# Kernel tuning notes

Measured on AMD Instinct MI355X. Metric: run time of the kernel, lower is better.

## Reference

```python
import jax, jax.numpy as jnp
import numpy as np


def gelu(x):
    # custom GELU classes in such repos typically implement the tanh approximation
    return jax.nn.gelu(x, approximate=True)


def setup_inputs() -> dict:
    key = jax.random.key(0)
    ks = jax.random.split(key, 16)
    B, N1, N2, D, H = 4, 1024, 1024, 256, 4
    prev = jax.random.normal(ks[0], (B, N1, D), dtype=jnp.float32)
    curr = jax.random.normal(ks[1], (B, N2, D), dtype=jnp.float32)
    edges = jax.random.randint(ks[2], (B, N1, N2), 0, 2).astype(jnp.int32)

    def lin(k, fan_in, fan_out):
        kw, kb = jax.random.split(k)
        s = 1.0 / np.sqrt(fan_in)
        W = jax.random.uniform(kw, (fan_in, fan_out), jnp.float32, -s, s)
        b = jax.random.uniform(kb, (fan_out,), jnp.float32, -s, s)
        return W, b

    W_pre, b_pre = lin(ks[3], D, 6)
    W_cur, b_cur = lin(ks[4], D, 6)
    W_fuse, b_fuse = lin(ks[5], 12, 4)
    W_ffn, b_ffn = lin(ks[6], 12, 8)
    W_fcc, b_fcc = lin(ks[7], 8, H)
    W_fcg, b_fcg = lin(ks[8], 8, D)
    return {"prev": prev, "curr": curr, "edges": edges,
            "W_pre": W_pre, "b_pre": b_pre, "W_cur": W_cur, "b_cur": b_cur,
            "W_fuse": W_fuse, "b_fuse": b_fuse, "W_ffn": W_ffn, "b_ffn": b_ffn,
            "W_fcc": W_fcc, "b_fcc": b_fcc, "W_fcg": W_fcg, "b_fcg": b_fcg}


def reference(prev, curr, edges, W_pre, b_pre, W_cur, b_cur,
              W_fuse, b_fuse, W_ffn, b_ffn, W_fcc, b_fcc, W_fcg, b_fcg):
    B, N1, D = prev.shape
    N2 = curr.shape[1]
    H = W_fcc.shape[1]
    Dh = D // H
    mask = edges != 0                                   # [B,N1,N2]

    bt_pre = prev @ W_pre + b_pre                       # [B,N1,6]
    bt_cur = curr @ W_cur + b_cur                       # [B,N2,6]
    pair = jnp.concatenate([
        jnp.broadcast_to(bt_pre[:, :, None, :], (B, N1, N2, 6)),
        jnp.broadcast_to(bt_cur[:, None, :, :], (B, N1, N2, 6))], axis=-1)
    c = gelu(pair) @ W_fuse + b_fuse                    # [B,N1,N2,4]
    c = jnp.where(mask[..., None], c, 0.0)

    e1 = (jnp.sum(edges, axis=1) + 1).astype(c.dtype)   # [B,N2]
    d = jnp.sum(c, axis=1)[:, None] / e1[:, None, :, None]
    d = jnp.broadcast_to(d, c.shape)
    e = jnp.broadcast_to(jnp.max(c, axis=1)[:, None], c.shape)
    fused = gelu(jnp.concatenate([c, d, e], axis=-1)) @ W_ffn + b_ffn  # [B,N1,N2,8]

    att = gelu(fused) @ W_fcc + b_fcc                   # [B,N1,N2,H]
    att = jnp.transpose(att, (0, 2, 1, 3))              # [B,N2,N1,H]
    maskT = jnp.transpose(mask, (0, 2, 1))              # [B,N2,N1]
    logits = jnp.where(maskT[..., None], att, -9e15)
    p = jax.nn.softmax(logits, axis=2)                  # softmax over N1 per head
    p = jnp.where(maskT[..., None], p, 0.0)
    # per-head aggregation: head i uses prev columns [i*Dh, (i+1)*Dh)
    res = jnp.einsum('bmnh,bnhd->bmhd', p, prev.reshape(B, N1, H, Dh)).reshape(B, N2, D)

    fused_m = jnp.where(mask[..., None], fused, 0.0)
    g = jnp.sum(fused_m, axis=1) / e1[..., None]        # [B,N2,8]
    return res + gelu(g) @ W_fcg + b_fcg                # [B,N2,D]
```

## Files before the change

kernel.cpp:

```cpp
#include <hip/hip_runtime.h>


using bf16x8 = __attribute__((ext_vector_type(8))) short;
using f32x4  = __attribute__((ext_vector_type(4))) float;
typedef float v2f __attribute__((ext_vector_type(2)));

__device__ __forceinline__ v2f pk_fma(v2f a, v2f b, v2f c){
    return __builtin_elementwise_fma(a, b, c);
}

__device__ __forceinline__ float gelu_f(float x){
    float x2 = x*x;
    float tt = x * __builtin_fmaf(0.044715f, x2, 1.0f);
    float e  = exp2f(-2.3022082f * tt);
    return x * __builtin_amdgcn_rcpf(1.0f + e);
}

__device__ __forceinline__ v2f gelu2(v2f x){
    v2f x2 = x*x;
    v2f tt = x * pk_fma((v2f){0.044715f,0.044715f}, x2, (v2f){1.0f,1.0f});
    float e0 = exp2f(-2.3022082f * tt[0]);
    float e1 = exp2f(-2.3022082f * tt[1]);
    v2f r = { __builtin_amdgcn_rcpf(1.0f + e0),
              __builtin_amdgcn_rcpf(1.0f + e1) };
    return x * r;
}

__device__ __forceinline__ unsigned short f2bf(float f){
    unsigned int u = __float_as_uint(f);
    u += 0x7FFFu + ((u >> 16) & 1u);
    return (unsigned short)(u >> 16);
}

__global__ __launch_bounds__(256) void k_prevT(
    const float* __restrict__ prev, unsigned short* __restrict__ prevT)
{
    int bid = blockIdx.x;
    int b  = bid >> 6;
    int it = (bid >> 2) & 15;
    int dt = bid & 3;
    int i0 = it*64, d0 = dt*64;
    int t = threadIdx.x;
    int col = t & 63, rw = t >> 6;
    __shared__ float tile[64][65];
    #pragma unroll
    for (int r = 0; r < 16; ++r){
        int row = rw + 4*r;
        tile[row][col] = prev[((size_t)b*1024 + i0 + row)*256 + d0 + col];
    }
    __syncthreads();
    #pragma unroll
    for (int r = 0; r < 16; ++r){
        int drow = rw + 4*r;
        prevT[((size_t)b*256 + d0 + drow)*1024 + i0 + col] = f2bf(tile[col][drow]);
    }
}

__global__ __launch_bounds__(256) void k_rows(
    const float* __restrict__ prev, const float* __restrict__ curr,
    const float* __restrict__ W_pre, const float* __restrict__ b_pre,
    const float* __restrict__ W_cur, const float* __restrict__ b_cur,
    const float* __restrict__ W_fuse, const float* __restrict__ b_fuse,
    float* __restrict__ u_ws, float* __restrict__ v_ws)
{
    int gid  = blockIdx.x * 256 + threadIdx.x;
    int wave = gid >> 6;
    int lane = threadIdx.x & 63;
    bool isPrev = wave < 4096;
    int row = isPrev ? wave : (wave - 4096);
    const float* xrow = (isPrev ? prev : curr) + (size_t)row * 256;
    const float* W  = isPrev ? W_pre : W_cur;
    const float* bv = isPrev ? b_pre : b_cur;

    float4 x4 = *reinterpret_cast<const float4*>(xrow + lane*4);
    const float* Wl = W + lane*24;
    float p[6];
    #pragma unroll
    for (int k=0;k<6;++k)
        p[k] = x4.x*Wl[k] + x4.y*Wl[6+k] + x4.z*Wl[12+k] + x4.w*Wl[18+k];
    #pragma unroll
    for (int off=32; off>=1; off>>=1){
        #pragma unroll
        for (int k=0;k<6;++k) p[k] += __shfl_xor(p[k], off, 64);
    }
    if (lane == 0){
        float g[6];
        #pragma unroll
        for(int k=0;k<6;++k) g[k] = gelu_f(p[k] + bv[k]);
        int rb = isPrev ? 0 : 6;
        float o[4];
        #pragma unroll
        for(int kk=0;kk<4;++kk){
            float a = isPrev ? 0.0f : b_fuse[kk];
            #pragma unroll
            for(int k=0;k<6;++k) a += g[k]*W_fuse[(rb+k)*4+kk];
            o[kk]=a;
        }
        float* dst = (isPrev ? u_ws : v_ws) + (size_t)row*4;
        *reinterpret_cast<float4*>(dst) = make_float4(o[0],o[1],o[2],o[3]);
    }
}

__global__ __launch_bounds__(256) void k_cols(
    const int* __restrict__ edges,
    const float* __restrict__ u_ws, const float* __restrict__ v_ws,
    const float* __restrict__ W_ffn, const float* __restrict__ b_ffn,
    float* __restrict__ Gd_ws, float* __restrict__ cnt_ws)
{
    int b  = blockIdx.x >> 6;
    int j0 = (blockIdx.x & 63) * 16;
    int t  = threadIdx.x;
    int jq = t & 3, sl = t >> 2;
    const int*   eb = edges + (size_t)b*1048576 + j0 + jq*4;
    const float* ub = u_ws + (size_t)b*4096;

    int   cnt[4] = {0,0,0,0};
    float S[4][4] = {{0.f}};
    float M[4][4];
    #pragma unroll
    for (int q=0;q<4;++q)
        #pragma unroll
        for (int k=0;k<4;++k) M[q][k] = -3.4e38f;

    #pragma unroll 4
    for (int ii=0; ii<16; ++ii){
        int i = sl*16 + ii;
        int4   e4 = *reinterpret_cast<const int4*>(eb + (size_t)i*1024);
        float4 u4 = *reinterpret_cast<const float4*>(ub + i*4);
        float uu[4] = {u4.x,u4.y,u4.z,u4.w};
        int   ee[4] = {e4.x,e4.y,e4.z,e4.w};
        #pragma unroll
        for (int q=0;q<4;++q){
            bool mk = ee[q]!=0;
            cnt[q] += mk ? 1 : 0;
            #pragma unroll
            for (int k=0;k<4;++k){
                S[q][k] += mk ? uu[k] : 0.0f;
                M[q][k]  = mk ? fmaxf(M[q][k],uu[k]) : M[q][k];
            }
        }
    }
    __shared__ float rS[64][16][4];
    __shared__ float rM[64][16][4];
    __shared__ int   rC[64][16];
    #pragma unroll
    for (int q=0;q<4;++q){
        int c = jq*4+q;
        #pragma unroll
        for (int k=0;k<4;++k){ rS[sl][c][k]=S[q][k]; rM[sl][c][k]=M[q][k]; }
        rC[sl][c]=cnt[q];
    }
    __syncthreads();
    float aS[4], aM[4]; int aC=0; int c2=0, hf=0;
    if (t < 128){
        c2 = t & 15; hf = t >> 4;
        #pragma unroll
        for(int k=0;k<4;++k){ aS[k]=0.f; aM[k]=-3.4e38f; }
        for (int s2=hf*8; s2<hf*8+8; ++s2){
            aC += rC[s2][c2];
            #pragma unroll
            for(int k=0;k<4;++k){ aS[k]+=rS[s2][c2][k]; aM[k]=fmaxf(aM[k],rM[s2][c2][k]); }
        }
    }
    __syncthreads();
    if (t < 128){
        rC[hf][c2]=aC;
        #pragma unroll
        for(int k=0;k<4;++k){ rS[hf][c2][k]=aS[k]; rM[hf][c2][k]=aM[k]; }
    }
    __syncthreads();
    if (t < 16){
        int cc=0; float Sa[4]={0,0,0,0};
        float Ma[4]={-3.4e38f,-3.4e38f,-3.4e38f,-3.4e38f};
        for (int s2=0;s2<8;++s2){
            cc += rC[s2][t];
            #pragma unroll
            for(int k=0;k<4;++k){ Sa[k]+=rS[s2][t][k]; Ma[k]=fmaxf(Ma[k],rM[s2][t][k]); }
        }
        size_t cj = (size_t)b*1024 + j0 + t;
        float4 v4 = *reinterpret_cast<const float4*>(v_ws + cj*4);
        float vv[4]={v4.x,v4.y,v4.z,v4.w};
        float cf = (float)cc, e1 = cf + 1.0f;
        float gd[4], ge[4];
        #pragma unroll
        for(int k=0;k<4;++k){
            float dk = (Sa[k] + cf*vv[k]) / e1;
            float ek;
            if (cc == 0) ek = 0.0f;
            else { float m1 = Ma[k]+vv[k]; ek = (cc < 1024) ? fmaxf(m1, 0.0f) : m1; }
            gd[k]=gelu_f(dk); ge[k]=gelu_f(ek);
        }
        #pragma unroll
        for(int kk=0;kk<8;++kk){
            float a = b_ffn[kk];
            #pragma unroll
            for(int k=0;k<4;++k)
                a += gd[k]*W_ffn[(4+k)*8+kk] + ge[k]*W_ffn[(8+k)*8+kk];
            Gd_ws[cj*8+kk]=a;
        }
        cnt_ws[cj]=cf;
    }
}

template<int SPLIT>
__global__ __launch_bounds__(256) void k_main(
    const unsigned short* __restrict__ prevT, const int* __restrict__ edges,
    const float* __restrict__ u_ws, const float* __restrict__ v_ws,
    const float* __restrict__ Gd_ws,
    const float* __restrict__ W_ffn, const float* __restrict__ W_fcc,
    const float* __restrict__ b_fcc,
    float* __restrict__ Pws, float* __restrict__ Sws, float* __restrict__ Tws)
{
    const int RPB = 1024/SPLIT;
    int bid = blockIdx.x;
    int sp  = bid & (SPLIT-1);
    int jt  = (bid / SPLIT) & 127;
    int b   = bid / (SPLIT*128);
    int j0  = jt*8;
    int t   = threadIdx.x;
    int lane = t & 63;
    int wv   = t >> 6;
    int jl_w = t & 7, il_w = t >> 3;

    __shared__ unsigned short wA[4096];
    __shared__ __align__(16) float sU[64][4];
    __shared__ float sV[8][4];
    __shared__ float sGd[8][8];
    __shared__ float sT4[256][4];

    if (t < 32) (&sV[0][0])[t]  = v_ws[((size_t)b*1024 + j0)*4 + t];
    if (t < 64) (&sGd[0][0])[t] = Gd_ws[((size_t)b*1024 + j0)*8 + t];
    {
        unsigned int* wz = (unsigned int*)wA;
        #pragma unroll
        for (int z=0; z<8; ++z) wz[t + z*256] = 0u;
    }

    const float LOG2E = 1.4426950408889634f;
    v2f W4p[4][4], Wfcp[8][2], bfcp[2];
    #pragma unroll
    for(int k=0;k<4;++k)
        #pragma unroll
        for(int q=0;q<4;++q)
            W4p[k][q] = (v2f){W_ffn[k*8+2*q], W_ffn[k*8+2*q+1]};
    #pragma unroll
    for(int kk=0;kk<8;++kk)
        #pragma unroll
        for(int p2=0;p2<2;++p2)
            Wfcp[kk][p2] = (v2f){W_fcc[kk*4+2*p2]*LOG2E, W_fcc[kk*4+2*p2+1]*LOG2E};
    #pragma unroll
    for(int p2=0;p2<2;++p2)
        bfcp[p2] = (v2f){b_fcc[2*p2]*LOG2E, b_fcc[2*p2+1]*LOG2E};

    f32x4 accm[4];
    #pragma unroll
    for (int tile=0;tile<4;++tile) accm[tile] = (f32x4){0.f,0.f,0.f,0.f};
    f32x4 accs = (f32x4){0.f,0.f,0.f,0.f};
    bf16x8 onesB;
    #pragma unroll
    for (int e=0;e<8;++e) onesB[e] = (short)0x3F80;
    v2f Tp01 = {0,0}, Tp23 = {0,0};

    const int* ebase = edges + (size_t)b*1048576 + j0;
    const int NCH = RPB/64;
    const int base_i0 = sp*RPB;

    __syncthreads();
    float4 v4p = *reinterpret_cast<const float4*>(&sV[jl_w][0]);
    float4 gd0 = *reinterpret_cast<const float4*>(&sGd[jl_w][0]);
    float4 gd1 = *reinterpret_cast<const float4*>(&sGd[jl_w][4]);

    int arow = lane & 15, kgrp = lane >> 4;
    int aoff0 = (((wv*16 + arow)*64 + kgrp*8)*2) ^ ((arow & 7) << 4);
    int aoff1 = aoff0 ^ 64;
    const unsigned short* pTbase = prevT
        + ((size_t)b*256 + wv*64 + arow)*1024 + base_i0 + kgrp*8;

    float su_r = u_ws[((size_t)b*1024 + base_i0)*4 + t];
    int   egr0 = ebase[(size_t)(base_i0+il_w   )*1024 + jl_w];
    int   egr1 = ebase[(size_t)(base_i0+il_w+32)*1024 + jl_w];

    for (int cc=0; cc<NCH; ++cc){
        (&sU[0][0])[t] = su_r;
        __syncthreads();

        int eg2[2] = {egr0, egr1};
        #pragma unroll
        for (int r=0;r<2;++r){
            int il = il_w + 32*r;
            int eg = eg2[r];
            float4 u4 = *reinterpret_cast<const float4*>(&sU[il][0]);
            v2f g01 = gelu2((v2f){u4.x + v4p.x, u4.y + v4p.y});
            v2f g23 = gelu2((v2f){u4.z + v4p.z, u4.w + v4p.w});
            float m = eg ? 1.0f : 0.0f;
            v2f mm = {m, m};
            Tp01 = pk_fma(mm, g01, Tp01);
            Tp23 = pk_fma(mm, g23, Tp23);
            v2f a0 = {gd0.x, gd0.y}, a1 = {gd0.z, gd0.w};
            v2f a2 = {gd1.x, gd1.y}, a3 = {gd1.z, gd1.w};
            v2f G0 = {g01[0], g01[0]}, G1 = {g01[1], g01[1]};
            v2f G2 = {g23[0], g23[0]}, G3 = {g23[1], g23[1]};
            a0 = pk_fma(G0, W4p[0][0], a0); a1 = pk_fma(G0, W4p[0][1], a1);
            a2 = pk_fma(G0, W4p[0][2], a2); a3 = pk_fma(G0, W4p[0][3], a3);
            a0 = pk_fma(G1, W4p[1][0], a0); a1 = pk_fma(G1, W4p[1][1], a1);
            a2 = pk_fma(G1, W4p[1][2], a2); a3 = pk_fma(G1, W4p[1][3], a3);
            a0 = pk_fma(G2, W4p[2][0], a0); a1 = pk_fma(G2, W4p[2][1], a1);
            a2 = pk_fma(G2, W4p[2][2], a2); a3 = pk_fma(G2, W4p[2][3], a3);
            a0 = pk_fma(G3, W4p[3][0], a0); a1 = pk_fma(G3, W4p[3][1], a1);
            a2 = pk_fma(G3, W4p[3][2], a2); a3 = pk_fma(G3, W4p[3][3], a3);
            v2f f01 = gelu2(a0), f23 = gelu2(a1);
            v2f f45 = gelu2(a2), f67 = gelu2(a3);
            v2f L01 = bfcp[0], L23 = bfcp[1];
            float fv[8] = {f01[0],f01[1],f23[0],f23[1],f45[0],f45[1],f67[0],f67[1]};
            #pragma unroll
            for (int kk=0;kk<8;++kk){
                v2f F = {fv[kk], fv[kk]};
                L01 = pk_fma(F, Wfcp[kk][0], L01);
                L23 = pk_fma(F, Wfcp[kk][1], L23);
            }
            float lg[4] = {L01[0], L01[1], L23[0], L23[1]};
            int low = ((jl_w*64 + il)*2) ^ (jl_w << 4);
            #pragma unroll
            for (int hh=0;hh<4;++hh){
                float wf = eg ? exp2f(lg[hh]) : 0.0f;
                *reinterpret_cast<unsigned short*>(
                    reinterpret_cast<char*>(wA) + hh*2048 + low) = f2bf(wf);
            }
        }

        {
            int i0n = base_i0 + ((cc+1 < NCH) ? (cc+1)*64 : 0);
            su_r = u_ws[((size_t)b*1024 + i0n)*4 + t];
            egr0 = ebase[(size_t)(i0n+il_w   )*1024 + jl_w];
            egr1 = ebase[(size_t)(i0n+il_w+32)*1024 + jl_w];
        }
        __syncthreads();

        bf16x8 afr0 = *reinterpret_cast<const bf16x8*>(
            reinterpret_cast<const char*>(wA) + aoff0);
        bf16x8 afr1 = *reinterpret_cast<const bf16x8*>(
            reinterpret_cast<const char*>(wA) + aoff1);
        const unsigned short* pT = pTbase + (size_t)cc*64;
        #pragma unroll
        for (int tile=0; tile<4; ++tile){
            const unsigned short* pB = pT + (size_t)tile*16*1024;
            bf16x8 bfr0 = *reinterpret_cast<const bf16x8*>(pB);
            bf16x8 bfr1 = *reinterpret_cast<const bf16x8*>(pB + 32);
            accm[tile] = __builtin_amdgcn_mfma_f32_16x16x32_bf16(
                afr0, bfr0, accm[tile], 0, 0, 0);
            accm[tile] = __builtin_amdgcn_mfma_f32_16x16x32_bf16(
                afr1, bfr1, accm[tile], 0, 0, 0);
        }
        accs = __builtin_amdgcn_mfma_f32_16x16x32_bf16(afr0, onesB, accs, 0,0,0);
        accs = __builtin_amdgcn_mfma_f32_16x16x32_bf16(afr1, onesB, accs, 0,0,0);
    }

    size_t bp = ((size_t)b*128 + jt)*SPLIT + sp;

    {
        float* ts = sT4[t];
        ts[0]=Tp01[0]; ts[1]=Tp01[1]; ts[2]=Tp23[0]; ts[3]=Tp23[1];
    }
    __syncthreads();
    if (t < 8){
        float T0=0,T1=0,T2=0,T3=0;
        for (int s2=0;s2<32;++s2){
            const float* p = sT4[s2*8 + t];
            T0+=p[0]; T1+=p[1]; T2+=p[2]; T3+=p[3];
        }
        float* td = Tws + (bp*8 + t)*4;
        td[0]=T0; td[1]=T1; td[2]=T2; td[3]=T3;
    }

    if (arow == 0 && kgrp < 2){
        #pragma unroll
        for (int r2=0; r2<4; ++r2)
            Sws[bp*32 + wv*8 + kgrp*4 + r2] = accs[r2];
    }
    if (kgrp < 2){
        #pragma unroll
        for (int tile=0; tile<4; ++tile){
            #pragma unroll
            for (int r2=0; r2<4; ++r2){
                int j   = kgrp*4 + r2;
                int dim = wv*64 + tile*16 + arow;
                Pws[((size_t)bp*8 + j)*256 + dim] = accm[tile][r2];
            }
        }
    }
}

template<int SPLIT>
__global__ __launch_bounds__(256) void k_merge(
    const float* __restrict__ Pws, const float* __restrict__ Sws,
    const float* __restrict__ Tws,
    const float* __restrict__ Gd_ws, const float* __restrict__ cnt_ws,
    const float* __restrict__ W_ffn, const float* __restrict__ W_fcg,
    const float* __restrict__ b_fcg, float* __restrict__ out)
{
    int b  = blockIdx.x >> 7;
    int jt = blockIdx.x & 127;
    int j0 = jt*8;
    int t  = threadIdx.x;
    int jl = t >> 5, hd = t & 31, h = hd >> 3, dq = hd & 7;
    __shared__ float sG[8][8];

    size_t bp0 = ((size_t)b*128 + jt)*SPLIT;
    float s = 0.0f, acc[8] = {0,0,0,0,0,0,0,0};
    #pragma unroll
    for (int sp2=0; sp2<SPLIT; ++sp2){
        const float* p = Pws + ((bp0+sp2)*8 + jl)*256 + hd*8;
        float4 p0 = *reinterpret_cast<const float4*>(p);
        float4 p1 = *reinterpret_cast<const float4*>(p+4);
        acc[0]+=p0.x; acc[1]+=p0.y; acc[2]+=p0.z; acc[3]+=p0.w;
        acc[4]+=p1.x; acc[5]+=p1.y; acc[6]+=p1.z; acc[7]+=p1.w;
        s += Sws[(bp0+sp2)*32 + h*8 + jl];
    }
    if (t < 8){
        float T[4] = {0,0,0,0};
        #pragma unroll
        for (int sp2=0; sp2<SPLIT; ++sp2){
            const float* tp = Tws + ((bp0+sp2)*8 + t)*4;
            #pragma unroll
            for (int k=0;k<4;++k) T[k]+=tp[k];
        }
        size_t cj = (size_t)b*1024 + j0 + t;
        float cf = cnt_ws[cj];
        float inv = __fdividef(1.0f, cf + 1.0f);
        #pragma unroll
        for (int kk=0;kk<8;++kk){
            float a = cf*Gd_ws[cj*8+kk];
            #pragma unroll
            for (int k=0;k<4;++k) a += T[k]*W_ffn[k*8+kk];
            sG[t][kk] = gelu_f(a*inv);
        }
    }
    __syncthreads();

    float rs = (s > 0.0f) ? (1.0f/s) : 0.0f;
    int col0 = h*64 + dq*8;
    float gg[8];
    #pragma unroll
    for (int kk=0;kk<8;++kk) gg[kk]=sG[jl][kk];
    float o[8];
    #pragma unroll
    for (int d2=0;d2<8;++d2){
        float a = b_fcg[col0+d2];
        #pragma unroll
        for (int kk=0;kk<8;++kk) a += gg[kk]*W_fcg[kk*256 + col0 + d2];
        o[d2] = acc[d2]*rs + a;
    }
    float* ob = out + ((size_t)b*1024 + j0 + jl)*256 + col0;
    float4* o4 = reinterpret_cast<float4*>(ob);
    o4[0] = make_float4(o[0],o[1],o[2],o[3]);
    o4[1] = make_float4(o[4],o[5],o[6],o[7]);
}

extern "C" void kernel_launch(void* const* d_in, const int* in_sizes, int n_in,
                              void* d_out, int out_size, void* d_ws, size_t ws_size,
                              hipStream_t stream)
{
    const float* prev  = (const float*)d_in[0];
    const float* curr  = (const float*)d_in[1];
    const int*   edges = (const int*)  d_in[2];
    const float* W_pre = (const float*)d_in[3];
    const float* b_pre = (const float*)d_in[4];
    const float* W_cur = (const float*)d_in[5];
    const float* b_cur = (const float*)d_in[6];
    const float* W_fuse= (const float*)d_in[7];
    const float* b_fuse= (const float*)d_in[8];
    const float* W_ffn = (const float*)d_in[9];
    const float* b_ffn = (const float*)d_in[10];
    const float* W_fcc = (const float*)d_in[11];
    const float* b_fcc = (const float*)d_in[12];
    const float* W_fcg = (const float*)d_in[13];
    const float* b_fcg = (const float*)d_in[14];
    float* out = (float*)d_out;

    float* u_ws   = (float*)d_ws;
    float* v_ws   = u_ws  + 16384;
    float* Gd_ws  = v_ws  + 16384;
    float* cnt_ws = Gd_ws + 32768;
    float* Pws    = cnt_ws + 4096;
    const size_t base_f = 16384 + 16384 + 32768 + 4096;

    const size_t p4  = (size_t)4*128*4*8*256;
    const size_t s4v = (size_t)4*128*4*32;
    const size_t t4  = (size_t)4*128*4*8*4;
    const size_t pT_f = (size_t)4*256*1024/2;
    const size_t need4 = (base_f + p4 + s4v + t4 + pT_f) * 4;
    const size_t p2 = p4/2, s2v = s4v/2, t2 = t4/2;
    const size_t need2 = (base_f + p2 + s2v + t2 + pT_f) * 4;
    const size_t p1 = p4/4, s1 = s4v/4, t1 = t4/4;

    k_rows<<<dim3(2048), dim3(256), 0, stream>>>(prev, curr, W_pre, b_pre,
        W_cur, b_cur, W_fuse, b_fuse, u_ws, v_ws);
    k_cols<<<dim3(256), dim3(256), 0, stream>>>(edges, u_ws, v_ws,
        W_ffn, b_ffn, Gd_ws, cnt_ws);

    if (ws_size >= need4){
        float* Sws = Pws + p4;
        float* Tws = Sws + s4v;
        unsigned short* prevT = (unsigned short*)(Tws + t4);
        k_prevT<<<dim3(256), dim3(256), 0, stream>>>(prev, prevT);
        k_main<4><<<dim3(2048), dim3(256), 0, stream>>>(prevT, edges, u_ws,
            v_ws, Gd_ws, W_ffn, W_fcc, b_fcc, Pws, Sws, Tws);
        k_merge<4><<<dim3(512), dim3(256), 0, stream>>>(Pws, Sws, Tws, Gd_ws,
            cnt_ws, W_ffn, W_fcg, b_fcg, out);
    } else if (ws_size >= need2){
        float* Sws = Pws + p2;
        float* Tws = Sws + s2v;
        unsigned short* prevT = (unsigned short*)(Tws + t2);
        k_prevT<<<dim3(256), dim3(256), 0, stream>>>(prev, prevT);
        k_main<2><<<dim3(1024), dim3(256), 0, stream>>>(prevT, edges, u_ws,
            v_ws, Gd_ws, W_ffn, W_fcc, b_fcc, Pws, Sws, Tws);
        k_merge<2><<<dim3(512), dim3(256), 0, stream>>>(Pws, Sws, Tws, Gd_ws,
            cnt_ws, W_ffn, W_fcg, b_fcg, out);
    } else {
        float* Sws = Pws + p1;
        float* Tws = Sws + s1;
        unsigned short* prevT = (unsigned short*)(Tws + t1);
        k_prevT<<<dim3(256), dim3(256), 0, stream>>>(prev, prevT);
        k_main<1><<<dim3(512), dim3(256), 0, stream>>>(prevT, edges, u_ws,
            v_ws, Gd_ws, W_ffn, W_fcc, b_fcc, Pws, Sws, Tws);
        k_merge<1><<<dim3(512), dim3(256), 0, stream>>>(Pws, Sws, Tws, Gd_ws,
            cnt_ws, W_ffn, W_fcg, b_fcg, out);
    }
}
```

Baseline: 74.91 us.

## Merge prevT transpose into row kernel and double-buffer main loop LDS

Merges the prev transpose/bf16 conversion kernel into the row-projection kernel as extra blocks, so there is one launch fewer and the two independent jobs run together. In the main kernel, the weight tile and u staging buffers in LDS are double-buffered, which removes one of the two barriers per chunk. Edge loads for the next chunk are issued earlier and u is prefetched two chunks ahead. The reduction scratch now reuses the weight buffer, which keeps LDS growth small, though the double buffers still raise LDS use and may reduce occupancy.

```diff
diff --git a/kernel.cpp b/kernel.cpp
--- a/kernel.cpp
+++ b/kernel.cpp
@@ -32,72 +32,72 @@
     return (unsigned short)(u >> 16);
 }
 
-__global__ __launch_bounds__(256) void k_prevT(
-    const float* __restrict__ prev, unsigned short* __restrict__ prevT)
-{
-    int bid = blockIdx.x;
-    int b  = bid >> 6;
-    int it = (bid >> 2) & 15;
-    int dt = bid & 3;
-    int i0 = it*64, d0 = dt*64;
-    int t = threadIdx.x;
-    int col = t & 63, rw = t >> 6;
-    __shared__ float tile[64][65];
-    #pragma unroll
-    for (int r = 0; r < 16; ++r){
-        int row = rw + 4*r;
-        tile[row][col] = prev[((size_t)b*1024 + i0 + row)*256 + d0 + col];
-    }
-    __syncthreads();
-    #pragma unroll
-    for (int r = 0; r < 16; ++r){
-        int drow = rw + 4*r;
-        prevT[((size_t)b*256 + d0 + drow)*1024 + i0 + col] = f2bf(tile[col][drow]);
-    }
-}
-
-__global__ __launch_bounds__(256) void k_rows(
+__global__ __launch_bounds__(256) void k_rowsT(
     const float* __restrict__ prev, const float* __restrict__ curr,
     const float* __restrict__ W_pre, const float* __restrict__ b_pre,
     const float* __restrict__ W_cur, const float* __restrict__ b_cur,
     const float* __restrict__ W_fuse, const float* __restrict__ b_fuse,
-    float* __restrict__ u_ws, float* __restrict__ v_ws)
+    float* __restrict__ u_ws, float* __restrict__ v_ws,
+    unsigned short* __restrict__ prevT)
 {
-    int gid  = blockIdx.x * 256 + threadIdx.x;
-    int wave = gid >> 6;
-    int lane = threadIdx.x & 63;
-    bool isPrev = wave < 4096;
-    int row = isPrev ? wave : (wave - 4096);
-    const float* xrow = (isPrev ? prev : curr) + (size_t)row * 256;
-    const float* W  = isPrev ? W_pre : W_cur;
-    const float* bv = isPrev ? b_pre : b_cur;
-
-    float4 x4 = *reinterpret_cast<const float4*>(xrow + lane*4);
-    const float* Wl = W + lane*24;
-    float p[6];
-    #pragma unroll
-    for (int k=0;k<6;++k)
-        p[k] = x4.x*Wl[k] + x4.y*Wl[6+k] + x4.z*Wl[12+k] + x4.w*Wl[18+k];
-    #pragma unroll
-    for (int off=32; off>=1; off>>=1){
-        #pragma unroll
-        for (int k=0;k<6;++k) p[k] += __shfl_xor(p[k], off, 64);
-    }
-    if (lane == 0){
-        float g[6];
-        #pragma unroll
-        for(int k=0;k<6;++k) g[k] = gelu_f(p[k] + bv[k]);
-        int rb = isPrev ? 0 : 6;
-        float o[4];
-        #pragma unroll
-        for(int kk=0;kk<4;++kk){
-            float a = isPrev ? 0.0f : b_fuse[kk];
-            #pragma unroll
-            for(int k=0;k<6;++k) a += g[k]*W_fuse[(rb+k)*4+kk];
-            o[kk]=a;
-        }
-        float* dst = (isPrev ? u_ws : v_ws) + (size_t)row*4;
-        *reinterpret_cast<float4*>(dst) = make_float4(o[0],o[1],o[2],o[3]);
+    __shared__ float tile[64][65];
+    int t = threadIdx.x;
+    if (blockIdx.x < 2048){
+        int gid  = blockIdx.x * 256 + t;
+        int wave = gid >> 6;
+        int lane = t & 63;
+        bool isPrev = wave < 4096;
+        int row = isPrev ? wave : (wave - 4096);
+        const float* xrow = (isPrev ? prev : curr) + (size_t)row * 256;
+        const float* W  = isPrev ? W_pre : W_cur;
+        const float* bv = isPrev ? b_pre : b_cur;
+
+        float4 x4 = *reinterpret_cast<const float4*>(xrow + lane*4);
+        const float* Wl = W + lane*24;
+        float p[6];
+        #pragma unroll
+        for (int k=0;k<6;++k)
+            p[k] = x4.x*Wl[k] + x4.y*Wl[6+k] + x4.z*Wl[12+k] + x4.w*Wl[18+k];
+        #pragma unroll
+        for (int off=32; off>=1; off>>=1){
+            #pragma unroll
+            for (int k=0;k<6;++k) p[k] += __shfl_xor(p[k], off, 64);
+        }
+        if (lane == 0){
+            float g[6];
+            #pragma unroll
+            for(int k=0;k<6;++k) g[k] = gelu_f(p[k] + bv[k]);
+            int rb = isPrev ? 0 : 6;
+            float o[4];
+            #pragma unroll
+            for(int kk=0;kk<4;++kk){
+                float a = isPrev ? 0.0f : b_fuse[kk];
+                #pragma unroll
+                for(int k=0;k<6;++k) a += g[k]*W_fuse[(rb+k)*4+kk];
+                o[kk]=a;
+            }
+            float* dst = (isPrev ? u_ws : v_ws) + (size_t)row*4;
+            *reinterpret_cast<float4*>(dst) = make_float4(o[0],o[1],o[2],o[3]);
+        }
+    } else {
+        int pbid = blockIdx.x - 2048;
+        int b  = pbid >> 6;
+        int it = (pbid >> 2) & 15;
+        int dt = pbid & 3;
+        int i0 = it*64, d0 = dt*64;
+        int col = t & 63, rw = t >> 6;
+        #pragma unroll
+        for (int r = 0; r < 16; ++r){
+            int row = rw + 4*r;
+            tile[row][col] = prev[((size_t)b*1024 + i0 + row)*256 + d0 + col];
+        }
+        __syncthreads();
+        #pragma unroll
+        for (int r = 0; r < 16; ++r){
+            int drow = rw + 4*r;
+            prevT[((size_t)b*256 + d0 + drow)*1024 + i0 + col]
+                = f2bf(tile[col][drow]);
+        }
     }
 }
 
@@ -222,18 +222,17 @@
     int wv   = t >> 6;
     int jl_w = t & 7, il_w = t >> 3;
 
-    __shared__ unsigned short wA[4096];
-    __shared__ __align__(16) float sU[64][4];
+    __shared__ unsigned short wA[2][4096];
+    __shared__ __align__(16) float sU[2][64][4];
     __shared__ float sV[8][4];
     __shared__ float sGd[8][8];
-    __shared__ float sT4[256][4];
 
     if (t < 32) (&sV[0][0])[t]  = v_ws[((size_t)b*1024 + j0)*4 + t];
     if (t < 64) (&sGd[0][0])[t] = Gd_ws[((size_t)b*1024 + j0)*8 + t];
     {
         unsigned int* wz = (unsigned int*)wA;
         #pragma unroll
-        for (int z=0; z<8; ++z) wz[t + z*256] = 0u;
+        for (int z=0; z<16; ++z) wz[t + z*256] = 0u;
     }
 
     const float LOG2E = 1.4426950408889634f;
@@ -264,11 +263,6 @@
     const int* ebase = edges + (size_t)b*1048576 + j0;
     const int NCH = RPB/64;
     const int base_i0 = sp*RPB;
-
-    __syncthreads();
-    float4 v4p = *reinterpret_cast<const float4*>(&sV[jl_w][0]);
-    float4 gd0 = *reinterpret_cast<const float4*>(&sGd[jl_w][0]);
-    float4 gd1 = *reinterpret_cast<const float4*>(&sGd[jl_w][4]);
 
     int arow = lane & 15, kgrp = lane >> 4;
     int aoff0 = (((wv*16 + arow)*64 + kgrp*8)*2) ^ ((arow & 7) << 4);
@@ -277,19 +271,35 @@
         + ((size_t)b*256 + wv*64 + arow)*1024 + base_i0 + kgrp*8;
 
     float su_r = u_ws[((size_t)b*1024 + base_i0)*4 + t];
-    int   egr0 = ebase[(size_t)(base_i0+il_w   )*1024 + jl_w];
-    int   egr1 = ebase[(size_t)(base_i0+il_w+32)*1024 + jl_w];
+    (&sU[0][0][0])[t] = su_r;
+    int egr0 = ebase[(size_t)(base_i0+il_w   )*1024 + jl_w];
+    int egr1 = ebase[(size_t)(base_i0+il_w+32)*1024 + jl_w];
+    {
+        int i0n = base_i0 + ((1 < NCH) ? 64 : 0);
+        su_r = u_ws[((size_t)b*1024 + i0n)*4 + t];
+    }
+    __syncthreads();
+
+    float4 v4p = *reinterpret_cast<const float4*>(&sV[jl_w][0]);
+    float4 gd0 = *reinterpret_cast<const float4*>(&sGd[jl_w][0]);
+    float4 gd1 = *reinterpret_cast<const float4*>(&sGd[jl_w][4]);
 
     for (int cc=0; cc<NCH; ++cc){
-        (&sU[0][0])[t] = su_r;
-        __syncthreads();
-
-        int eg2[2] = {egr0, egr1};
+        int p = cc & 1;
+        char* wAp = reinterpret_cast<char*>(wA) + p*8192;
+
+        int eg_c[2] = {egr0, egr1};
+        {
+            int i0n = base_i0 + ((cc+1 < NCH) ? (cc+1)*64 : 0);
+            egr0 = ebase[(size_t)(i0n+il_w   )*1024 + jl_w];
+            egr1 = ebase[(size_t)(i0n+il_w+32)*1024 + jl_w];
+        }
+
         #pragma unroll
         for (int r=0;r<2;++r){
             int il = il_w + 32*r;
-            int eg = eg2[r];
-            float4 u4 = *reinterpret_cast<const float4*>(&sU[il][0]);
+            int eg = eg_c[r];
+            float4 u4 = *reinterpret_cast<const float4*>(&sU[p][il][0]);
             v2f g01 = gelu2((v2f){u4.x + v4p.x, u4.y + v4p.y});
             v2f g23 = gelu2((v2f){u4.z + v4p.z, u4.w + v4p.w});
             float m = eg ? 1.0f : 0.0f;
@@ -323,23 +333,19 @@
             #pragma unroll
             for (int hh=0;hh<4;++hh){
                 float wf = eg ? exp2f(lg[hh]) : 0.0f;
-                *reinterpret_cast<unsigned short*>(
-                    reinterpret_cast<char*>(wA) + hh*2048 + low) = f2bf(wf);
+                *reinterpret_cast<unsigned short*>(wAp + hh*2048 + low) = f2bf(wf);
             }
         }
 
+        (&sU[p^1][0][0])[t] = su_r;
         {
-            int i0n = base_i0 + ((cc+1 < NCH) ? (cc+1)*64 : 0);
-            su_r = u_ws[((size_t)b*1024 + i0n)*4 + t];
-            egr0 = ebase[(size_t)(i0n+il_w   )*1024 + jl_w];
-            egr1 = ebase[(size_t)(i0n+il_w+32)*1024 + jl_w];
+            int i0n2 = base_i0 + ((cc+2 < NCH) ? (cc+2)*64 : 0);
+            su_r = u_ws[((size_t)b*1024 + i0n2)*4 + t];
         }
         __syncthreads();
 
-        bf16x8 afr0 = *reinterpret_cast<const bf16x8*>(
-            reinterpret_cast<const char*>(wA) + aoff0);
-        bf16x8 afr1 = *reinterpret_cast<const bf16x8*>(
-            reinterpret_cast<const char*>(wA) + aoff1);
+        bf16x8 afr0 = *reinterpret_cast<const bf16x8*>(wAp + aoff0);
+        bf16x8 afr1 = *reinterpret_cast<const bf16x8*>(wAp + aoff1);
         const unsigned short* pT = pTbase + (size_t)cc*64;
         #pragma unroll
         for (int tile=0; tile<4; ++tile){
@@ -357,15 +363,16 @@
 
     size_t bp = ((size_t)b*128 + jt)*SPLIT + sp;
 
+    float* sT4 = reinterpret_cast<float*>(wA);
     {
-        float* ts = sT4[t];
+        float* ts = sT4 + (size_t)t*4;
         ts[0]=Tp01[0]; ts[1]=Tp01[1]; ts[2]=Tp23[0]; ts[3]=Tp23[1];
     }
     __syncthreads();
     if (t < 8){
         float T0=0,T1=0,T2=0,T3=0;
         for (int s2=0;s2<32;++s2){
-            const float* p = sT4[s2*8 + t];
+            const float* p = sT4 + (size_t)(s2*8 + t)*4;
             T0+=p[0]; T1+=p[1]; T2+=p[2]; T3+=p[3];
         }
         float* td = Tws + (bp*8 + t)*4;
@@ -493,16 +500,14 @@
     const size_t need2 = (base_f + p2 + s2v + t2 + pT_f) * 4;
     const size_t p1 = p4/4, s1 = s4v/4, t1 = t4/4;
 
-    k_rows<<<dim3(2048), dim3(256), 0, stream>>>(prev, curr, W_pre, b_pre,
-        W_cur, b_cur, W_fuse, b_fuse, u_ws, v_ws);
-    k_cols<<<dim3(256), dim3(256), 0, stream>>>(edges, u_ws, v_ws,
-        W_ffn, b_ffn, Gd_ws, cnt_ws);
-
     if (ws_size >= need4){
         float* Sws = Pws + p4;
         float* Tws = Sws + s4v;
         unsigned short* prevT = (unsigned short*)(Tws + t4);
-        k_prevT<<<dim3(256), dim3(256), 0, stream>>>(prev, prevT);
+        k_rowsT<<<dim3(2304), dim3(256), 0, stream>>>(prev, curr, W_pre, b_pre,
+            W_cur, b_cur, W_fuse, b_fuse, u_ws, v_ws, prevT);
+        k_cols<<<dim3(256), dim3(256), 0, stream>>>(edges, u_ws, v_ws,
+            W_ffn, b_ffn, Gd_ws, cnt_ws);
         k_main<4><<<dim3(2048), dim3(256), 0, stream>>>(prevT, edges, u_ws,
             v_ws, Gd_ws, W_ffn, W_fcc, b_fcc, Pws, Sws, Tws);
         k_merge<4><<<dim3(512), dim3(256), 0, stream>>>(Pws, Sws, Tws, Gd_ws,
@@ -511,7 +516,10 @@
         float* Sws = Pws + p2;
         float* Tws = Sws + s2v;
         unsigned short* prevT = (unsigned short*)(Tws + t2);
-        k_prevT<<<dim3(256), dim3(256), 0, stream>>>(prev, prevT);
+        k_rowsT<<<dim3(2304), dim3(256), 0, stream>>>(prev, curr, W_pre, b_pre,
+            W_cur, b_cur, W_fuse, b_fuse, u_ws, v_ws, prevT);
+        k_cols<<<dim3(256), dim3(256), 0, stream>>>(edges, u_ws, v_ws,
+            W_ffn, b_ffn, Gd_ws, cnt_ws);
         k_main<2><<<dim3(1024), dim3(256), 0, stream>>>(prevT, edges, u_ws,
             v_ws, Gd_ws, W_ffn, W_fcc, b_fcc, Pws, Sws, Tws);
         k_merge<2><<<dim3(512), dim3(256), 0, stream>>>(Pws, Sws, Tws, Gd_ws,
@@ -520,7 +528,10 @@
         float* Sws = Pws + p1;
         float* Tws = Sws + s1;
         unsigned short* prevT = (unsigned short*)(Tws + t1);
-        k_prevT<<<dim3(256), dim3(256), 0, stream>>>(prev, prevT);
+        k_rowsT<<<dim3(2304), dim3(256), 0, stream>>>(prev, curr, W_pre, b_pre,
+            W_cur, b_cur, W_fuse, b_fuse, u_ws, v_ws, prevT);
+        k_cols<<<dim3(256), dim3(256), 0, stream>>>(edges, u_ws, v_ws,
+            W_ffn, b_ffn, Gd_ws, cnt_ws);
         k_main<1><<<dim3(512), dim3(256), 0, stream>>>(prevT, edges, u_ws,
             v_ws, Gd_ws, W_ffn, W_fcc, b_fcc, Pws, Sws, Tws);
         k_merge<1><<<dim3(512), dim3(256), 0, stream>>>(Pws, Sws, Tws, Gd_ws,
```

After: 74.36 us. No clear change (-0.7%).
